# Optimization experiments

Hardware: AMD Instinct MI355X
Metric: run time of the kernel (lower is better)

Reference implementation:

```python
import jax, jax.numpy as jnp
import numpy as np

FP8_E4M3_MAX = 448.0
F32_TINY = np.float32(np.finfo(np.float32).tiny)


def setup_inputs() -> dict:
    key = jax.random.key(0)
    k1, k2, k3, k4 = jax.random.split(key, 4)
    B, S, D_IN, D_OUT, BLK = 4, 2048, 4096, 4096, 128
    x = jax.random.normal(k1, (B, S, D_IN), dtype=jnp.float32)
    # Simulated fp8 weight values (post-quantization codes stored as f32) and
    # per-(row, in-block) scales, as produced by a blockwise weight quantizer.
    weight_fp8 = jax.random.normal(k2, (D_OUT, D_IN), dtype=jnp.float32)
    weight_scale = jax.random.uniform(k3, (D_OUT, D_IN // BLK), dtype=jnp.float32, minval=1e-3, maxval=1.0)
    bias = jax.random.normal(k4, (D_OUT,), dtype=jnp.float32)
    return {"x": x, "weight_fp8": weight_fp8, "weight_scale": weight_scale, "bias": bias, "blk": BLK}


def reference(x, weight_fp8, weight_scale, bias, blk):
    orig_dtype = x.dtype
    x32 = x.astype(jnp.float32)
    *batch_dims, last = x32.shape
    leading = int(np.prod(batch_dims)) if batch_dims else 1
    nblk = last // blk
    blocks = x32.reshape(leading, nblk, blk)             # [T, nblk, blk]
    amax = jnp.max(jnp.abs(blocks), axis=-1)             # [T, nblk]
    x_scales = jnp.maximum(amax / FP8_E4M3_MAX, F32_TINY)
    # pow2 rounding of activation scales (use_activation_pow2_scale=True)
    x_scales = jnp.exp2(jnp.round(jnp.log2(jnp.maximum(x_scales, F32_TINY))))
    s = x_scales[..., None]
    x_dq = ((blocks / s) * s).reshape(leading, last)     # quantize-emulate then dequant
    # weight dequant: bf16 scale broadcast over in-dim blocks
    w_scale = weight_scale.astype(jnp.bfloat16).astype(jnp.float32)  # [O, nblk]
    w_dq = (weight_fp8.reshape(weight_fp8.shape[0], nblk, blk) * w_scale[:, :, None]).reshape(weight_fp8.shape)
    y = x_dq @ w_dq.T + bias[None, :]                    # [T, O]
    return y.reshape(*batch_dims, -1).astype(orig_dtype)
```

## Files before the change

kernel.cpp:

```cpp
#include <hip/hip_runtime.h>
#include <cstdint>
#include <cstddef>


typedef __attribute__((ext_vector_type(8))) __bf16 bf16x8;
typedef __attribute__((ext_vector_type(4))) float f32x4;

__device__ __forceinline__ unsigned short bf16rn(float f) {
  unsigned u = __builtin_bit_cast(unsigned, f);
  u = (u + 0x7FFFu + ((u >> 16) & 1u)) >> 16;
  return (unsigned short)u;
}
__device__ __forceinline__ float bf16tof(unsigned short h) {
  unsigned u = ((unsigned)h) << 16;
  return __builtin_bit_cast(float, u);
}
__device__ __forceinline__ void gload_lds16(const void* g, void* l) {
  __builtin_amdgcn_global_load_lds(
      (const __attribute__((address_space(1))) unsigned int*)g,
      (__attribute__((address_space(3))) unsigned int*)l, 16, 0, 0);
}


__global__ __launch_bounds__(256) void k_prep(
    const float* __restrict__ x, const float* __restrict__ w,
    const float* __restrict__ sc, unsigned short* __restrict__ xb,
    unsigned short* __restrict__ wb, int K, int nblk, int blk,
    int n8x, int n8w) {
  int t = blockIdx.x * 256 + threadIdx.x;
  if (t < n8x) {
    const float4* p = (const float4*)x + (size_t)t * 2;
    float4 a = p[0], b = p[1];
    uint4 o;
    o.x = (unsigned)bf16rn(a.x) | ((unsigned)bf16rn(a.y) << 16);
    o.y = (unsigned)bf16rn(a.z) | ((unsigned)bf16rn(a.w) << 16);
    o.z = (unsigned)bf16rn(b.x) | ((unsigned)bf16rn(b.y) << 16);
    o.w = (unsigned)bf16rn(b.z) | ((unsigned)bf16rn(b.w) << 16);
    ((uint4*)xb)[t] = o;
  } else if (t - n8x < n8w) {
    int tw = t - n8x;
    size_t base = (size_t)tw * 8;
    int o_row = (int)(base / (size_t)K);
    int k = (int)(base % (size_t)K);
    float s = bf16tof(bf16rn(sc[(size_t)o_row * nblk + k / blk]));
    const float4* p = (const float4*)w + (size_t)tw * 2;
    float4 a = p[0], b = p[1];
    uint4 o;
    o.x = (unsigned)bf16rn(a.x * s) | ((unsigned)bf16rn(a.y * s) << 16);
    o.y = (unsigned)bf16rn(a.z * s) | ((unsigned)bf16rn(a.w * s) << 16);
    o.z = (unsigned)bf16rn(b.x * s) | ((unsigned)bf16rn(b.y * s) << 16);
    o.w = (unsigned)bf16rn(b.z * s) | ((unsigned)bf16rn(b.w * s) << 16);
    ((uint4*)wb)[tw] = o;
  }
}


#define BM 256
#define BN 256
#define BK 64

#define BARF()                                  \
  do {                                          \
    __builtin_amdgcn_s_barrier();               \
    asm volatile("" ::: "memory");              \
    __builtin_amdgcn_sched_barrier(0);          \
  } while (0)
#define WAIT_VM(n) asm volatile("s_waitcnt vmcnt(" #n ")" ::: "memory")
#define WAIT_LGKM(n) asm volatile("s_waitcnt lgkmcnt(" #n ")" ::: "memory")
#define SCHEDB() __builtin_amdgcn_sched_barrier(0)
#define PRIO(p) __builtin_amdgcn_s_setprio(p)

#define STG_A(buf, q, tile)                                               \
  gload_lds16(Ag + (size_t)(q) * 64 * Ks + (size_t)(tile) * BK,           \
              smem + (buf) * 65536 + (q) * 8192 + tid16)
#define STG_B(buf, q, tile)                                               \
  gload_lds16(Bg + (size_t)(q) * 64 * Ks + (size_t)(tile) * BK,           \
              smem + (buf) * 65536 + 32768 + (q) * 8192 + tid16)

#define READ_A(arr, buf, qm)                                              \
  _Pragma("unroll") for (int i_ = 0; i_ < 4; ++i_) {                      \
    arr[i_][0] = *(const bf16x8*)(smem + (buf) * 65536 +                  \
        (wr * 128 + (qm) * 64 + i_ * 16 + lr) * 128 + ko0);               \
    arr[i_][1] = *(const bf16x8*)(smem + (buf) * 65536 +                  \
        (wr * 128 + (qm) * 64 + i_ * 16 + lr) * 128 + ko1);               \
  }
#define READ_B(arr, buf, qn)                                              \
  _Pragma("unroll") for (int j_ = 0; j_ < 2; ++j_) {                      \
    arr[j_][0] = *(const bf16x8*)(smem + (buf) * 65536 + 32768 +          \
        (wc * 64 + (qn) * 32 + j_ * 16 + lr) * 128 + ko0);                \
    arr[j_][1] = *(const bf16x8*)(smem + (buf) * 65536 + 32768 +          \
        (wc * 64 + (qn) * 32 + j_ * 16 + lr) * 128 + ko1);                \
  }
#define MFMA_Q(qm, qn, aarr, barr)                                        \
  _Pragma("unroll") for (int kk_ = 0; kk_ < 2; ++kk_)                     \
  _Pragma("unroll") for (int i_ = 0; i_ < 4; ++i_)                        \
  _Pragma("unroll") for (int j_ = 0; j_ < 2; ++j_)                        \
    acc[(qm) * 4 + i_][(qn) * 2 + j_] =                                   \
        __builtin_amdgcn_mfma_f32_16x16x32_bf16(                          \
            aarr[i_][kk_], barr[j_][kk_],                                 \
            acc[(qm) * 4 + i_][(qn) * 2 + j_], 0, 0, 0);

__global__ __launch_bounds__(512, 2) void k_gemm256(
    const unsigned short* __restrict__ A, const unsigned short* __restrict__ B,
    const float* __restrict__ bias, float* __restrict__ C,
    int M, int N, int K) {
  extern __shared__ __align__(16) char smem[];

  const int nbn = N / BN;
  const int nwg = gridDim.x;
  int bid = blockIdx.x;
  int wg = bid;
  if ((nwg & 7) == 0) wg = (bid & 7) * (nwg >> 3) + (bid >> 3);
  const int m0 = (wg / nbn) * BM;
  const int n0 = (wg % nbn) * BN;

  const int tid = threadIdx.x;
  const int lane = tid & 63;
  const int wid = tid >> 6;
  const int wr = wid >> 2;
  const int wc = wid & 3;
  const int lr = lane & 15;
  const int ko0 = (((lane >> 4) * 16) ^ ((lane & 7) << 4));
  const int ko1 = ((64 | ((lane >> 4) * 16)) ^ ((lane & 7) << 4));
  const int tid16 = tid * 16;

  const int srow = tid >> 3;
  const int sgran = (tid & 7) ^ (srow & 7);
  const size_t Ks = (size_t)K;
  const unsigned short* Ag = A + (size_t)(m0 + srow) * Ks + sgran * 8;
  const unsigned short* Bg = B + (size_t)(n0 + srow) * Ks + sgran * 8;

  f32x4 acc[8][4] = {};
  bf16x8 a0[4][2], a1[4][2], b0[2][2], b1[2][2];

  const int NT = K / BK;
  const int NITER = NT / 2;

  STG_A(0, 0, 0); STG_A(0, 2, 0); STG_A(0, 1, 0); STG_A(0, 3, 0);
  STG_B(0, 0, 0); STG_B(0, 2, 0); STG_B(0, 1, 0); STG_B(0, 3, 0);
  STG_A(1, 0, 1); STG_A(1, 2, 1);
  STG_B(1, 0, 1); STG_B(1, 2, 1);
  STG_A(1, 1, 1); STG_A(1, 3, 1);
  WAIT_VM(6);
  BARF();

  for (int it = 0; it < NITER; ++it) {
    const int t = 2 * it;
    const bool s2 = (t + 2) < NT;
    const bool s3 = (t + 3) < NT;
    READ_A(a0, 0, 0); READ_B(b0, 0, 0);
    STG_B(1, 1, t + 1); STG_B(1, 3, t + 1);
    SCHEDB(); WAIT_LGKM(8);
    BARF();
    WAIT_LGKM(0); SCHEDB();
    PRIO(1); MFMA_Q(0, 0, a0, b0); PRIO(0);
    BARF();
    READ_B(b1, 0, 1);
    if (s2) { STG_A(0, 0, t + 2); STG_A(0, 2, t + 2); }
    SCHEDB();
    BARF();
    WAIT_LGKM(0); SCHEDB();
    PRIO(1); MFMA_Q(0, 1, a0, b1); PRIO(0);
    BARF();
    READ_A(a1, 0, 1);
    if (s2) { STG_B(0, 0, t + 2); STG_B(0, 2, t + 2); }
    SCHEDB();
    BARF();
    WAIT_LGKM(0); SCHEDB();
    PRIO(1); MFMA_Q(1, 0, a1, b0); PRIO(0);
    BARF();
    if (s2) { STG_A(0, 1, t + 2); STG_A(0, 3, t + 2); WAIT_VM(6); }
    else    { WAIT_VM(0); }
    BARF();
    PRIO(1); MFMA_Q(1, 1, a1, b1); PRIO(0);
    BARF();
    READ_A(a0, 1, 0); READ_B(b0, 1, 0);
    if (s2) { STG_B(0, 1, t + 2); STG_B(0, 3, t + 2); }
    SCHEDB(); WAIT_LGKM(8);
    BARF();
    WAIT_LGKM(0); SCHEDB();
    PRIO(1); MFMA_Q(0, 0, a0, b0); PRIO(0);
    BARF();
    READ_B(b1, 1, 1);
    if (s3) { STG_A(1, 0, t + 3); STG_A(1, 2, t + 3); }
    SCHEDB();
    BARF();
    WAIT_LGKM(0); SCHEDB();
    PRIO(1); MFMA_Q(0, 1, a0, b1); PRIO(0);
    BARF();
    READ_A(a1, 1, 1);
    if (s3) { STG_B(1, 0, t + 3); STG_B(1, 2, t + 3); }
    SCHEDB();
    BARF();
    WAIT_LGKM(0); SCHEDB();
    PRIO(1); MFMA_Q(1, 0, a1, b0); PRIO(0);
    BARF();
    if (s3) { STG_A(1, 1, t + 3); STG_A(1, 3, t + 3); WAIT_VM(6); }
    else if (s2) { WAIT_VM(0); }
    BARF();
    PRIO(1); MFMA_Q(1, 1, a1, b1); PRIO(0);
    BARF();
  }

  const int col0 = n0 + wc * 64 + (lane & 15);
  const int row0 = m0 + wr * 128 + ((lane >> 4) << 2);
  float bj[4];
#pragma unroll
  for (int j = 0; j < 4; ++j) bj[j] = bias[col0 + j * 16];
#pragma unroll
  for (int i = 0; i < 8; ++i) {
#pragma unroll
    for (int r = 0; r < 4; ++r) {
      const size_t ro = (size_t)(row0 + i * 16 + r) * N;
#pragma unroll
      for (int j = 0; j < 4; ++j) {
        C[ro + col0 + j * 16] = acc[i][j][r] + bj[j];
      }
    }
  }
}


__global__ __launch_bounds__(256) void k_fallback(
    const float* __restrict__ x, const float* __restrict__ w,
    const float* __restrict__ sc, const float* __restrict__ bias,
    float* __restrict__ out, int T, int O, int K, int nblk, int blk) {
  long long idx = (long long)blockIdx.x * 256 + threadIdx.x;
  if (idx >= (long long)T * O) return;
  int row = (int)(idx / O), col = (int)(idx % O);
  const float* xr = x + (size_t)row * K;
  const float* wr = w + (size_t)col * K;
  const float* sr = sc + (size_t)col * nblk;
  float acc = 0.f;
  for (int b = 0; b < nblk; ++b) {
    float s = bf16tof(bf16rn(sr[b]));
    float part = 0.f;
    for (int k = 0; k < blk; k += 4) {
      float4 xa = *(const float4*)(xr + b * blk + k);
      float4 wa = *(const float4*)(wr + b * blk + k);
      part += xa.x * wa.x + xa.y * wa.y + xa.z * wa.z + xa.w * wa.w;
    }
    acc += part * s;
  }
  out[idx] = acc + bias[col];
}

extern "C" void kernel_launch(void* const* d_in, const int* in_sizes, int n_in,
                              void* d_out, int out_size, void* d_ws, size_t ws_size,
                              hipStream_t stream) {
  const float* x = (const float*)d_in[0];
  const float* w = (const float*)d_in[1];
  const float* sc = (const float*)d_in[2];
  const float* bias = (const float*)d_in[3];
  float* out = (float*)d_out;

  const int x_n = in_sizes[0];
  const int w_n = in_sizes[1];
  const int s_n = in_sizes[2];
  const int O = in_sizes[3];
  const int K = w_n / O;
  const int T = x_n / K;
  const int nblk = s_n / O;
  const int blk = K / nblk;

  const size_t need = (size_t)x_n * 2 + (size_t)w_n * 2;
  const bool tiled_ok = ws_size >= need && (K % (2 * BK)) == 0 &&
                        (T % BM) == 0 && (O % BN) == 0 && (blk % 8) == 0 &&
                        K >= 2 * BK;

  if (tiled_ok) {
    unsigned short* xb = (unsigned short*)d_ws;
    unsigned short* wb = xb + (size_t)x_n;
    int n8x = x_n / 8, n8w = w_n / 8;
    int nprep = n8x + n8w;
    k_prep<<<(nprep + 255) / 256, 256, 0, stream>>>(x, w, sc, xb, wb, K, nblk,
                                                    blk, n8x, n8w);
    hipFuncSetAttribute((const void*)k_gemm256,
                        hipFuncAttributeMaxDynamicSharedMemorySize, 131072);
    dim3 grid((T / BM) * (O / BN));
    k_gemm256<<<grid, 512, 131072, stream>>>(xb, wb, bias, out, T, O, K);
  } else {
    long long total = (long long)T * O;
    dim3 grid((unsigned)((total + 255) / 256));
    k_fallback<<<grid, 256, 0, stream>>>(x, w, sc, bias, out, T, O, K, nblk, blk);
  }
}
```

Baseline: 284.8 us.

## Software-pipeline LDS fragment reads one MFMA quadrant ahead of compute

Restructures the main GEMM loop so each LDS read of the next A/B fragments is issued before the MFMA quadrant that uses the previous fragments. The LDS wait and barrier move to after the MFMA, and the first fragments are preloaded before the loop. This halves the number of barriers per quadrant and hides LDS read latency behind matrix math. In exchange it changes the global-load wait counts and the s3 guard is replaced by s2, which assumes NT is even, and it relies on the register fragments not being overwritten early.

```diff
diff --git a/kernel.cpp b/kernel.cpp
--- a/kernel.cpp
+++ b/kernel.cpp
@@ -143,62 +143,56 @@
   STG_A(1, 1, 1); STG_A(1, 3, 1);
   WAIT_VM(6);
   BARF();
+  READ_A(a0, 0, 0); READ_B(b0, 0, 0);
 
   for (int it = 0; it < NITER; ++it) {
     const int t = 2 * it;
     const bool s2 = (t + 2) < NT;
-    const bool s3 = (t + 3) < NT;
-    READ_A(a0, 0, 0); READ_B(b0, 0, 0);
+    READ_B(b1, 0, 1);
     STG_B(1, 1, t + 1); STG_B(1, 3, t + 1);
-    SCHEDB(); WAIT_LGKM(8);
-    BARF();
-    WAIT_LGKM(0); SCHEDB();
+    SCHEDB();
     PRIO(1); MFMA_Q(0, 0, a0, b0); PRIO(0);
-    BARF();
-    READ_B(b1, 0, 1);
+    WAIT_LGKM(0);
+    BARF();
+    READ_A(a1, 0, 1);
     if (s2) { STG_A(0, 0, t + 2); STG_A(0, 2, t + 2); }
     SCHEDB();
-    BARF();
-    WAIT_LGKM(0); SCHEDB();
     PRIO(1); MFMA_Q(0, 1, a0, b1); PRIO(0);
-    BARF();
-    READ_A(a1, 0, 1);
+    WAIT_LGKM(0);
+    BARF();
     if (s2) { STG_B(0, 0, t + 2); STG_B(0, 2, t + 2); }
     SCHEDB();
-    BARF();
-    WAIT_LGKM(0); SCHEDB();
     PRIO(1); MFMA_Q(1, 0, a1, b0); PRIO(0);
-    BARF();
-    if (s2) { STG_A(0, 1, t + 2); STG_A(0, 3, t + 2); WAIT_VM(6); }
-    else    { WAIT_VM(0); }
-    BARF();
+    if (s2) { WAIT_VM(4); } else { WAIT_VM(0); }
+    BARF();
+    READ_A(a0, 1, 0); READ_B(b0, 1, 0);
+    if (s2) { STG_A(0, 1, t + 2); STG_A(0, 3, t + 2); }
+    SCHEDB();
     PRIO(1); MFMA_Q(1, 1, a1, b1); PRIO(0);
-    BARF();
-    READ_A(a0, 1, 0); READ_B(b0, 1, 0);
+    WAIT_LGKM(0);
+    BARF();
+    READ_B(b1, 1, 1);
     if (s2) { STG_B(0, 1, t + 2); STG_B(0, 3, t + 2); }
-    SCHEDB(); WAIT_LGKM(8);
-    BARF();
-    WAIT_LGKM(0); SCHEDB();
+    SCHEDB();
     PRIO(1); MFMA_Q(0, 0, a0, b0); PRIO(0);
-    BARF();
-    READ_B(b1, 1, 1);
-    if (s3) { STG_A(1, 0, t + 3); STG_A(1, 2, t + 3); }
-    SCHEDB();
-    BARF();
-    WAIT_LGKM(0); SCHEDB();
+    WAIT_LGKM(0);
+    BARF();
+    READ_A(a1, 1, 1);
+    if (s2) { STG_A(1, 0, t + 3); STG_A(1, 2, t + 3); }
+    SCHEDB();
     PRIO(1); MFMA_Q(0, 1, a0, b1); PRIO(0);
-    BARF();
-    READ_A(a1, 1, 1);
-    if (s3) { STG_B(1, 0, t + 3); STG_B(1, 2, t + 3); }
-    SCHEDB();
-    BARF();
-    WAIT_LGKM(0); SCHEDB();
+    WAIT_LGKM(0);
+    BARF();
+    if (s2) { STG_B(1, 0, t + 3); STG_B(1, 2, t + 3); }
+    SCHEDB();
     PRIO(1); MFMA_Q(1, 0, a1, b0); PRIO(0);
-    BARF();
-    if (s3) { STG_A(1, 1, t + 3); STG_A(1, 3, t + 3); WAIT_VM(6); }
-    else if (s2) { WAIT_VM(0); }
-    BARF();
+    if (s2) { WAIT_VM(4); }
+    BARF();
+    if (s2) { READ_A(a0, 0, 0); READ_B(b0, 0, 0); }
+    if (s2) { STG_A(1, 1, t + 3); STG_A(1, 3, t + 3); }
+    SCHEDB();
     PRIO(1); MFMA_Q(1, 1, a1, b1); PRIO(0);
+    WAIT_LGKM(0);
     BARF();
   }
 
```

Result: slower. 613.4 us (+115.4%).
